# Performance work log

Measured on AMD Instinct MI355X. Metric: run time of the kernel, lower is better.

## Reference

```python
import jax, jax.numpy as jnp
import numpy as np

DIM = 128
POS_HID = 64
ATTN_HID = DIM * 4
K_NEIGH = 16


def _mlp2(x, w1, b1, w2, b2):
    # Linear -> ReLU -> Linear (weights stored as (in, out))
    return jax.nn.relu(x @ w1 + b1) @ w2 + b2


def setup_inputs() -> dict:
    key = jax.random.key(0)
    ks = jax.random.split(key, 12)
    B, N = 2, 512
    s = 0.05
    return {
        "x": jax.random.normal(ks[0], (B, DIM, N), jnp.float32),
        "pos": jax.random.normal(ks[1], (B, N, 3), jnp.float32),
        "w_qkv": jax.random.normal(ks[2], (DIM, 3 * DIM), jnp.float32) * s,
        "pos_w1": jax.random.normal(ks[3], (3, POS_HID), jnp.float32) * s,
        "pos_b1": jnp.zeros((POS_HID,), jnp.float32),
        "pos_w2": jax.random.normal(ks[4], (POS_HID, DIM), jnp.float32) * s,
        "pos_b2": jnp.zeros((DIM,), jnp.float32),
        "attn_w1": jax.random.normal(ks[5], (DIM, ATTN_HID), jnp.float32) * s,
        "attn_b1": jnp.zeros((ATTN_HID,), jnp.float32),
        "attn_w2": jax.random.normal(ks[6], (ATTN_HID, DIM), jnp.float32) * s,
        "attn_b2": jnp.zeros((DIM,), jnp.float32),
    }


def reference(x, pos, w_qkv, pos_w1, pos_b1, pos_w2, pos_b2,
              attn_w1, attn_b1, attn_w2, attn_b2):
    # x: (B, dim, N) -> (B, N, dim)
    xt = jnp.swapaxes(x, 1, 2)
    B, N, d = xt.shape

    qkv = xt @ w_qkv                           # (B, N, 3d), no bias
    q, k, v = jnp.split(qkv, 3, axis=-1)

    rel_pos = pos[:, :, None, :] - pos[:, None, :, :]          # (B, N, N, 3)
    rel_pos_emb = _mlp2(rel_pos, pos_w1, pos_b1, pos_w2, pos_b2)  # (B, N, N, d)
    qk_rel = q[:, :, None, :] - k[:, None, :, :]               # (B, N, N, d)

    # KNN: smallest euclidean rel distances per query point
    rel_dist = jnp.sqrt(jnp.sum(rel_pos * rel_pos, axis=-1))   # (B, N, N)
    _, idx = jax.lax.top_k(-rel_dist, K_NEIGH)                 # (B, N, K)

    idxe = idx[..., None]                                      # (B, N, K, 1)
    v_g = v[jnp.arange(B)[:, None, None], idx]                 # (B, N, K, d)
    qk_g = jnp.take_along_axis(qk_rel, idxe, axis=2)           # (B, N, K, d)
    pe_g = jnp.take_along_axis(rel_pos_emb, idxe, axis=2)      # (B, N, K, d)

    v_g = v_g + pe_g
    sim = _mlp2(qk_g + pe_g, attn_w1, attn_b1, attn_w2, attn_b2)  # (B, N, K, d)
    attn = jax.nn.softmax(sim, axis=-2)                        # softmax over neighbors
    agg = jnp.einsum('bikd,bikd->bid', attn, v_g)              # (B, N, d)
    return jnp.swapaxes(agg, 1, 2)                             # (B, d, N)
```

## Files before the change

kernel.cpp:

```cpp
#include <hip/hip_runtime.h>
#include <math.h>

#define DIM 128
#define N_PTS 512
#define K_NEIGH 16
#define POS_HID 64
#define ATTN_HID 512

typedef __attribute__((ext_vector_type(8))) short short8;
typedef __attribute__((ext_vector_type(4))) float f32x4;
typedef unsigned short us;
typedef unsigned long long ull;

__device__ __forceinline__ us f2b(float f) {
    unsigned int u = __builtin_bit_cast(unsigned int, f);
    u += 0x7fffu + ((u >> 16) & 1u);
    return (us)(u >> 16);
}

__device__ __forceinline__ ull shflx64(ull v, int m) {
    int lo = __shfl_xor((int)(unsigned int)v, m);
    int hi = __shfl_xor((int)(unsigned int)(v >> 32), m);
    return ((ull)(unsigned int)hi << 32) | (unsigned int)lo;
}

__global__ void pack_kernel(const float* __restrict__ wqkv,
                            const float* __restrict__ aw1,
                            const float* __restrict__ aw2,
                            const float* __restrict__ pw2,
                            us* __restrict__ p0, us* __restrict__ p1,
                            us* __restrict__ p2, us* __restrict__ p3) {
    int t = blockIdx.x * 256 + threadIdx.x;
    if (t < 49152) {
        int j = t & 7, l = (t >> 3) & 63, rem = t >> 9;
        int nt = rem % 24, ks = rem / 24;
        int k = ks * 32 + (l >> 4) * 8 + j, n = nt * 16 + (l & 15);
        p0[t] = f2b(wqkv[k * 384 + n]);
    } else if (t < 114688) {
        int u = t - 49152;
        int j = u & 7, l = (u >> 3) & 63, nt = (u >> 9) & 31, ks = u >> 14;
        int k = ks * 32 + (l >> 4) * 8 + j, n = nt * 16 + (l & 15);
        p1[u] = f2b(aw1[k * ATTN_HID + n]);
    } else if (t < 180224) {
        int u = t - 114688;
        int j = u & 7, l = (u >> 3) & 63, nt = (u >> 9) & 7, ch = u >> 12;
        int k = ch * 32 + (l >> 4) * 8 + j, n = nt * 16 + (l & 15);
        p2[u] = f2b(aw2[k * DIM + n]);
    } else if (t < 188416) {
        int u = t - 180224;
        int j = u & 7, l = (u >> 3) & 63, nt = (u >> 9) & 7, ks = u >> 12;
        int k = ks * 32 + (l >> 4) * 8 + j, n = nt * 16 + (l & 15);
        p3[u] = f2b(pw2[k * DIM + n]);
    }
}

__global__ __launch_bounds__(512)
void qkv_mfma_kernel(const float* __restrict__ x,
                     const us* __restrict__ p0,
                     float* __restrict__ qkv) {
    __shared__ __align__(16) us xA[16][136];
    const int tid = threadIdx.x;
    const int w = tid >> 6, lane = tid & 63, quad = lane >> 4, lq = lane & 15;
    const int n0 = blockIdx.x * 16;
    const int b = n0 >> 9, nn = n0 & (N_PTS - 1);
#pragma unroll
    for (int rr = 0; rr < 4; ++rr) {
        int id = rr * 512 + tid;
        int d = id >> 4, i = id & 15;
        xA[i][d] = f2b(x[(size_t)(b * DIM + d) * N_PTS + nn + i]);
    }
    __syncthreads();
    short8 a[4];
#pragma unroll
    for (int ks = 0; ks < 4; ++ks)
        a[ks] = *(const short8*)&xA[lq][ks * 32 + quad * 8];
#pragma unroll
    for (int i = 0; i < 3; ++i) {
        int nt = w * 3 + i;
        f32x4 acc = {0.f, 0.f, 0.f, 0.f};
#pragma unroll
        for (int ks = 0; ks < 4; ++ks) {
            const short8 bf = *(const short8*)(p0 + (size_t)((ks * 24 + nt) * 64 + lane) * 8);
            acc = __builtin_amdgcn_mfma_f32_16x16x32_bf16(a[ks], bf, acc, 0, 0, 0);
        }
#pragma unroll
        for (int r = 0; r < 4; ++r)
            qkv[(size_t)(n0 + quad * 4 + r) * 384 + nt * 16 + lq] = acc[r];
    }
}

__global__ __launch_bounds__(256, 1)
void attn_fused_kernel(const float* __restrict__ pos,
                       const float* __restrict__ qkv,
                       const float* __restrict__ pw1,
                       const float* __restrict__ pb1,
                       const float* __restrict__ pb2,
                       const us* __restrict__ p1,
                       const us* __restrict__ p2,
                       const us* __restrict__ p3,
                       const float* __restrict__ ab1,
                       float* __restrict__ out) {
    __shared__ __align__(16) us hinA[4][16][136];
    __shared__ __align__(16) us h1s[4][16][40];
    __shared__ int nbrs[4][16];

    const int tid = threadIdx.x;
    const int w = tid >> 6, lane = tid & 63, quad = lane >> 4, lq = lane & 15;
    const int g = blockIdx.x * 4 + w, b = g >> 9, n = g & (N_PTS - 1);

    short8 b3f[2][8];
#pragma unroll
    for (int ks = 0; ks < 2; ++ks)
#pragma unroll
        for (int nt = 0; nt < 8; ++nt)
            b3f[ks][nt] = *(const short8*)(p3 + (size_t)((ks * 8 + nt) * 64 + lane) * 8);

    float w1x[2][8], w1y[2][8], w1z[2][8], w1b[2][8];
#pragma unroll
    for (int ks = 0; ks < 2; ++ks)
#pragma unroll
        for (int jj = 0; jj < 8; ++jj) {
            int c = ks * 32 + quad * 8 + jj;
            w1x[ks][jj] = pw1[c];
            w1y[ks][jj] = pw1[64 + c];
            w1z[ks][jj] = pw1[128 + c];
            w1b[ks][jj] = pb1[c];
        }

    float qvr[8], pb2r[8], ab1r[32];
#pragma unroll
    for (int nt = 0; nt < 8; ++nt) {
        qvr[nt]  = qkv[(size_t)g * 384 + nt * 16 + lq];
        pb2r[nt] = pb2[nt * 16 + lq];
    }
#pragma unroll
    for (int nt = 0; nt < 32; ++nt) ab1r[nt] = ab1[nt * 16 + lq];

    {
        const float pix = pos[g * 3 + 0], piy = pos[g * 3 + 1], piz = pos[g * 3 + 2];
        float d2[8];
#pragma unroll
        for (int rr = 0; rr < 8; ++rr) {
            int j = rr * 64 + lane;
            float dx = pix - pos[(b * N_PTS + j) * 3 + 0];
            float dy = piy - pos[(b * N_PTS + j) * 3 + 1];
            float dz = piz - pos[(b * N_PTS + j) * 3 + 2];
            d2[rr] = dx * dx + dy * dy + dz * dz;
        }
        for (int r = 0; r < K_NEIGH; ++r) {
            ull key = ~0ULL;
#pragma unroll
            for (int rr = 0; rr < 8; ++rr) {
                unsigned int fb = __builtin_bit_cast(unsigned int, d2[rr]);
                ull k2 = ((ull)fb << 32) | (unsigned int)(rr * 64 + lane);
                key = k2 < key ? k2 : key;
            }
#pragma unroll
            for (int off = 32; off > 0; off >>= 1) {
                ull o = shflx64(key, off);
                key = o < key ? o : key;
            }
            unsigned int jw = (unsigned int)key;
            if (lane == 0) nbrs[w][r] = (int)jw;
            if (lane == (int)(jw & 63)) d2[jw >> 6] = __builtin_inff();
        }
    }

    short8 pha[2];
    {
        const int jn = nbrs[w][lq];
        float rx = pos[g * 3 + 0] - pos[(b * N_PTS + jn) * 3 + 0];
        float ry = pos[g * 3 + 1] - pos[(b * N_PTS + jn) * 3 + 1];
        float rz = pos[g * 3 + 2] - pos[(b * N_PTS + jn) * 3 + 2];
#pragma unroll
        for (int ks = 0; ks < 2; ++ks) {
            short8 f;
#pragma unroll
            for (int jj = 0; jj < 8; ++jj) {
                float h = rx * w1x[ks][jj] + ry * w1y[ks][jj] + rz * w1z[ks][jj] + w1b[ks][jj];
                f[jj] = (short)f2b(fmaxf(h, 0.f));
            }
            pha[ks] = f;
        }
    }

    f32x4 pe[8];
#pragma unroll
    for (int nt = 0; nt < 8; ++nt) {
        f32x4 acc = {0.f, 0.f, 0.f, 0.f};
        acc = __builtin_amdgcn_mfma_f32_16x16x32_bf16(pha[0], b3f[0][nt], acc, 0, 0, 0);
        acc = __builtin_amdgcn_mfma_f32_16x16x32_bf16(pha[1], b3f[1][nt], acc, 0, 0, 0);
#pragma unroll
        for (int r = 0; r < 4; ++r) pe[nt][r] = acc[r] + pb2r[nt];
    }

    f32x4 vg[8];
    {
        int jr[4];
#pragma unroll
        for (int r = 0; r < 4; ++r) jr[r] = nbrs[w][quad * 4 + r];
#pragma unroll
        for (int nt = 0; nt < 8; ++nt) {
            int d = nt * 16 + lq;
#pragma unroll
            for (int r = 0; r < 4; ++r) {
                const float* kv = qkv + (size_t)(b * N_PTS + jr[r]) * 384;
                float pp = pe[nt][r];
                hinA[w][quad * 4 + r][d] = f2b(qvr[nt] - kv[128 + d] + pp);
                vg[nt][r] = kv[256 + d] + pp;
            }
        }
    }

    short8 a1f[4];
#pragma unroll
    for (int ks = 0; ks < 4; ++ks)
        a1f[ks] = *(const short8*)&hinA[w][lq][ks * 32 + quad * 8];

    f32x4 c2[8];
#pragma unroll
    for (int nt = 0; nt < 8; ++nt) c2[nt] = (f32x4){0.f, 0.f, 0.f, 0.f};

    short8 p1f[2][2][4];
    short8 p2f[2][8];
#pragma unroll
    for (int t = 0; t < 2; ++t)
#pragma unroll
        for (int ks = 0; ks < 4; ++ks)
            p1f[0][t][ks] = *(const short8*)(p1 + (size_t)(((ks << 5) + t) * 64 + lane) * 8);
#pragma unroll
    for (int nt2 = 0; nt2 < 8; ++nt2)
        p2f[0][nt2] = *(const short8*)(p2 + (size_t)(nt2 * 64 + lane) * 8);

#pragma unroll
    for (int ch = 0; ch < 16; ++ch) {
        const int cur = ch & 1, nxt = cur ^ 1;
        if (ch < 15) {
#pragma unroll
            for (int t = 0; t < 2; ++t)
#pragma unroll
                for (int ks = 0; ks < 4; ++ks)
                    p1f[nxt][t][ks] = *(const short8*)(p1 + (size_t)(((ks << 5) + (ch + 1) * 2 + t) * 64 + lane) * 8);
        }
#pragma unroll
        for (int t = 0; t < 2; ++t) {
            int nt = ch * 2 + t;
            f32x4 acc = {0.f, 0.f, 0.f, 0.f};
#pragma unroll
            for (int ks = 0; ks < 4; ++ks)
                acc = __builtin_amdgcn_mfma_f32_16x16x32_bf16(a1f[ks], p1f[cur][t][ks], acc, 0, 0, 0);
            float bias = ab1r[nt];
#pragma unroll
            for (int r = 0; r < 4; ++r)
                h1s[w][quad * 4 + r][t * 16 + lq] = f2b(fmaxf(acc[r] + bias, 0.f));
        }
        if (ch < 15) {
#pragma unroll
            for (int nt2 = 0; nt2 < 8; ++nt2)
                p2f[nxt][nt2] = *(const short8*)(p2 + (size_t)((((ch + 1) << 3) + nt2) * 64 + lane) * 8);
        }
        const short8 a2 = *(const short8*)&h1s[w][lq][quad * 8];
#pragma unroll
        for (int nt2 = 0; nt2 < 8; ++nt2)
            c2[nt2] = __builtin_amdgcn_mfma_f32_16x16x32_bf16(a2, p2f[cur][nt2], c2[nt2], 0, 0, 0);
    }

#pragma unroll
    for (int nt2 = 0; nt2 < 8; ++nt2) {
        f32x4 s4 = c2[nt2];
        float m = fmaxf(fmaxf(s4[0], s4[1]), fmaxf(s4[2], s4[3]));
        m = fmaxf(m, __shfl_xor(m, 16));
        m = fmaxf(m, __shfl_xor(m, 32));
        float e0 = __expf(s4[0] - m), e1 = __expf(s4[1] - m);
        float e2 = __expf(s4[2] - m), e3 = __expf(s4[3] - m);
        float s = e0 + e1 + e2 + e3;
        f32x4 v4 = vg[nt2];
        float a = e0 * v4[0] + e1 * v4[1] + e2 * v4[2] + e3 * v4[3];
        s += __shfl_xor(s, 16); s += __shfl_xor(s, 32);
        a += __shfl_xor(a, 16); a += __shfl_xor(a, 32);
        if (quad == 0)
            out[(size_t)(b * DIM + nt2 * 16 + lq) * N_PTS + n] = a / s;
    }
}

extern "C" void kernel_launch(void* const* d_in, const int* in_sizes, int n_in,
                              void* d_out, int out_size, void* d_ws, size_t ws_size,
                              hipStream_t stream) {
    const float* x    = (const float*)d_in[0];
    const float* pos  = (const float*)d_in[1];
    const float* wqkv = (const float*)d_in[2];
    const float* pw1  = (const float*)d_in[3];
    const float* pb1  = (const float*)d_in[4];
    const float* pw2  = (const float*)d_in[5];
    const float* pb2  = (const float*)d_in[6];
    const float* aw1  = (const float*)d_in[7];
    const float* ab1  = (const float*)d_in[8];
    const float* aw2  = (const float*)d_in[9];
    float* out = (float*)d_out;

    int B = in_sizes[0] / (DIM * N_PTS);
    int npts = B * N_PTS;

    char* ws = (char*)d_ws;
    float* qkv = (float*)ws;
    us* p0 = (us*)(ws + (size_t)npts * 384 * 4);
    us* p1 = p0 + 49152;
    us* p2 = p1 + 65536;
    us* p3 = p2 + 65536;

    pack_kernel<<<736, 256, 0, stream>>>(wqkv, aw1, aw2, pw2, p0, p1, p2, p3);
    qkv_mfma_kernel<<<npts / 16, 512, 0, stream>>>(x, p0, qkv);
    attn_fused_kernel<<<npts / 4, 256, 0, stream>>>(pos, qkv,
                                                    pw1, pb1, pb2,
                                                    p1, p2, p3, ab1, out);
}
```

Measured before the change: 100.1 us.

## Split attention MLP hidden dimension across wave pairs with LDS reduction

Each point is now handled by two waves instead of one. Each wave computes half of the 512-wide hidden layer of the attention MLP, and the partial second-layer accumulators are exchanged through shared memory after a block barrier. Each wave then does the softmax and aggregation for half of the output channels. The grid doubles and launch bounds allow two blocks per CU, which aims to shorten the serial MFMA chain per wave and raise occupancy. The cost is that KNN selection and positional-embedding work are repeated in both waves, the register double-buffered weight prefetch is removed, and a __syncthreads plus LDS traffic is added.

```diff
diff --git a/kernel.cpp b/kernel.cpp
--- a/kernel.cpp
+++ b/kernel.cpp
@@ -89,7 +89,7 @@
     }
 }
 
-__global__ __launch_bounds__(256, 1)
+__global__ __launch_bounds__(256, 2)
 void attn_fused_kernel(const float* __restrict__ pos,
                        const float* __restrict__ qkv,
                        const float* __restrict__ pw1,
@@ -103,10 +103,13 @@
     __shared__ __align__(16) us hinA[4][16][136];
     __shared__ __align__(16) us h1s[4][16][40];
     __shared__ int nbrs[4][16];
+    __shared__ __align__(16) f32x4 cxch[4][4][64];
 
     const int tid = threadIdx.x;
     const int w = tid >> 6, lane = tid & 63, quad = lane >> 4, lq = lane & 15;
-    const int g = blockIdx.x * 4 + w, b = g >> 9, n = g & (N_PTS - 1);
+    const int pt = w >> 1, sub = w & 1;
+    const int g = blockIdx.x * 2 + pt, b = g >> 9, n = g & (N_PTS - 1);
+    const int ch0 = sub << 3;
 
     short8 b3f[2][8];
 #pragma unroll
@@ -127,14 +130,14 @@
             w1b[ks][jj] = pb1[c];
         }
 
-    float qvr[8], pb2r[8], ab1r[32];
+    float qvr[8], pb2r[8], ab1r[16];
 #pragma unroll
     for (int nt = 0; nt < 8; ++nt) {
         qvr[nt]  = qkv[(size_t)g * 384 + nt * 16 + lq];
         pb2r[nt] = pb2[nt * 16 + lq];
     }
 #pragma unroll
-    for (int nt = 0; nt < 32; ++nt) ab1r[nt] = ab1[nt * 16 + lq];
+    for (int i = 0; i < 16; ++i) ab1r[i] = ab1[(sub * 16 + i) * 16 + lq];
 
     {
         const float pix = pos[g * 3 + 0], piy = pos[g * 3 + 1], piz = pos[g * 3 + 2];
@@ -221,53 +224,48 @@
 #pragma unroll
     for (int nt = 0; nt < 8; ++nt) c2[nt] = (f32x4){0.f, 0.f, 0.f, 0.f};
 
-    short8 p1f[2][2][4];
-    short8 p2f[2][8];
-#pragma unroll
-    for (int t = 0; t < 2; ++t)
-#pragma unroll
-        for (int ks = 0; ks < 4; ++ks)
-            p1f[0][t][ks] = *(const short8*)(p1 + (size_t)(((ks << 5) + t) * 64 + lane) * 8);
-#pragma unroll
-    for (int nt2 = 0; nt2 < 8; ++nt2)
-        p2f[0][nt2] = *(const short8*)(p2 + (size_t)(nt2 * 64 + lane) * 8);
-
-#pragma unroll
-    for (int ch = 0; ch < 16; ++ch) {
-        const int cur = ch & 1, nxt = cur ^ 1;
-        if (ch < 15) {
-#pragma unroll
-            for (int t = 0; t < 2; ++t)
-#pragma unroll
-                for (int ks = 0; ks < 4; ++ks)
-                    p1f[nxt][t][ks] = *(const short8*)(p1 + (size_t)(((ks << 5) + (ch + 1) * 2 + t) * 64 + lane) * 8);
-        }
+#pragma unroll
+    for (int c = 0; c < 8; ++c) {
+        const int ch = ch0 + c;
+        short8 p1f[2][4];
+#pragma unroll
+        for (int t = 0; t < 2; ++t)
+#pragma unroll
+            for (int ks = 0; ks < 4; ++ks)
+                p1f[t][ks] = *(const short8*)(p1 + (size_t)(((ks << 5) + ch * 2 + t) * 64 + lane) * 8);
 #pragma unroll
         for (int t = 0; t < 2; ++t) {
-            int nt = ch * 2 + t;
             f32x4 acc = {0.f, 0.f, 0.f, 0.f};
 #pragma unroll
             for (int ks = 0; ks < 4; ++ks)
-                acc = __builtin_amdgcn_mfma_f32_16x16x32_bf16(a1f[ks], p1f[cur][t][ks], acc, 0, 0, 0);
-            float bias = ab1r[nt];
+                acc = __builtin_amdgcn_mfma_f32_16x16x32_bf16(a1f[ks], p1f[t][ks], acc, 0, 0, 0);
+            float bias = ab1r[c * 2 + t];
 #pragma unroll
             for (int r = 0; r < 4; ++r)
                 h1s[w][quad * 4 + r][t * 16 + lq] = f2b(fmaxf(acc[r] + bias, 0.f));
         }
-        if (ch < 15) {
-#pragma unroll
-            for (int nt2 = 0; nt2 < 8; ++nt2)
-                p2f[nxt][nt2] = *(const short8*)(p2 + (size_t)((((ch + 1) << 3) + nt2) * 64 + lane) * 8);
-        }
+        short8 p2f[8];
+#pragma unroll
+        for (int nt2 = 0; nt2 < 8; ++nt2)
+            p2f[nt2] = *(const short8*)(p2 + (size_t)(((ch << 3) + nt2) * 64 + lane) * 8);
         const short8 a2 = *(const short8*)&h1s[w][lq][quad * 8];
 #pragma unroll
         for (int nt2 = 0; nt2 < 8; ++nt2)
-            c2[nt2] = __builtin_amdgcn_mfma_f32_16x16x32_bf16(a2, p2f[cur][nt2], c2[nt2], 0, 0, 0);
-    }
-
-#pragma unroll
-    for (int nt2 = 0; nt2 < 8; ++nt2) {
+            c2[nt2] = __builtin_amdgcn_mfma_f32_16x16x32_bf16(a2, p2f[nt2], c2[nt2], 0, 0, 0);
+    }
+
+#pragma unroll
+    for (int i = 0; i < 4; ++i)
+        cxch[w][i][lane] = c2[(sub ^ 1) * 4 + i];
+    __syncthreads();
+
+#pragma unroll
+    for (int i = 0; i < 4; ++i) {
+        const int nt2 = sub * 4 + i;
+        f32x4 o = cxch[w ^ 1][i][lane];
         f32x4 s4 = c2[nt2];
+        s4[0] += o[0]; s4[1] += o[1]; s4[2] += o[2]; s4[3] += o[3];
+
         float m = fmaxf(fmaxf(s4[0], s4[1]), fmaxf(s4[2], s4[3]));
         m = fmaxf(m, __shfl_xor(m, 16));
         m = fmaxf(m, __shfl_xor(m, 32));
@@ -310,7 +308,7 @@
 
     pack_kernel<<<736, 256, 0, stream>>>(wqkv, aw1, aw2, pw2, p0, p1, p2, p3);
     qkv_mfma_kernel<<<npts / 16, 512, 0, stream>>>(x, p0, qkv);
-    attn_fused_kernel<<<npts / 4, 256, 0, stream>>>(pos, qkv,
+    attn_fused_kernel<<<npts / 2, 256, 0, stream>>>(pos, qkv,
                                                     pw1, pb1, pb2,
                                                     p1, p2, p3, ab1, out);
 }
```

New measurement: 111.4 us. 1.11x slower.

## Merge pack, QKV and attention kernels into one persistent kernel with grid barriers

Applied to the files above, without the earlier changes.

Replaces three separate launches (weight packing, QKV MFMA GEMM, fused attention) with a single kernel of npts/4 blocks that runs each phase in turn, separated by atomic-counter grid barriers. The aim is to remove launch gaps and inter-kernel drain between phases. The QKV work is redistributed so that four blocks share a 16-point tile, each computing six of the output column tiles. The grid barrier assumes all 256 blocks are co-resident, which holds on a 256-CU device with one block per CU but risks deadlock otherwise. It also adds a memset launch to reset the counters.

```diff
diff --git a/kernel.cpp b/kernel.cpp
--- a/kernel.cpp
+++ b/kernel.cpp
@@ -24,88 +24,103 @@
     return ((ull)(unsigned int)hi << 32) | (unsigned int)lo;
 }
 
-__global__ void pack_kernel(const float* __restrict__ wqkv,
-                            const float* __restrict__ aw1,
-                            const float* __restrict__ aw2,
-                            const float* __restrict__ pw2,
-                            us* __restrict__ p0, us* __restrict__ p1,
-                            us* __restrict__ p2, us* __restrict__ p3) {
-    int t = blockIdx.x * 256 + threadIdx.x;
-    if (t < 49152) {
-        int j = t & 7, l = (t >> 3) & 63, rem = t >> 9;
-        int nt = rem % 24, ks = rem / 24;
-        int k = ks * 32 + (l >> 4) * 8 + j, n = nt * 16 + (l & 15);
-        p0[t] = f2b(wqkv[k * 384 + n]);
-    } else if (t < 114688) {
-        int u = t - 49152;
-        int j = u & 7, l = (u >> 3) & 63, nt = (u >> 9) & 31, ks = u >> 14;
-        int k = ks * 32 + (l >> 4) * 8 + j, n = nt * 16 + (l & 15);
-        p1[u] = f2b(aw1[k * ATTN_HID + n]);
-    } else if (t < 180224) {
-        int u = t - 114688;
-        int j = u & 7, l = (u >> 3) & 63, nt = (u >> 9) & 7, ch = u >> 12;
-        int k = ch * 32 + (l >> 4) * 8 + j, n = nt * 16 + (l & 15);
-        p2[u] = f2b(aw2[k * DIM + n]);
-    } else if (t < 188416) {
-        int u = t - 180224;
-        int j = u & 7, l = (u >> 3) & 63, nt = (u >> 9) & 7, ks = u >> 12;
-        int k = ks * 32 + (l >> 4) * 8 + j, n = nt * 16 + (l & 15);
-        p3[u] = f2b(pw2[k * DIM + n]);
-    }
-}
-
-__global__ __launch_bounds__(512)
-void qkv_mfma_kernel(const float* __restrict__ x,
-                     const us* __restrict__ p0,
-                     float* __restrict__ qkv) {
+__device__ __forceinline__ void gbar(int* cnt, int target) {
+    __syncthreads();
+    if (threadIdx.x == 0) {
+        __hip_atomic_fetch_add(cnt, 1, __ATOMIC_RELEASE, __HIP_MEMORY_SCOPE_AGENT);
+        while (__hip_atomic_load(cnt, __ATOMIC_ACQUIRE, __HIP_MEMORY_SCOPE_AGENT) < target)
+            __builtin_amdgcn_s_sleep(2);
+    }
+    __syncthreads();
+}
+
+__global__ __launch_bounds__(256, 1)
+void fused_kernel(const float* __restrict__ x,
+                  const float* __restrict__ pos,
+                  const float* __restrict__ wqkv,
+                  const float* __restrict__ pw1,
+                  const float* __restrict__ pb1,
+                  const float* __restrict__ pw2,
+                  const float* __restrict__ pb2,
+                  const float* __restrict__ aw1,
+                  const float* __restrict__ ab1,
+                  const float* __restrict__ aw2,
+                  float* __restrict__ qkv,
+                  us* __restrict__ p0, us* __restrict__ p1,
+                  us* __restrict__ p2, us* __restrict__ p3,
+                  int* __restrict__ bar,
+                  float* __restrict__ out, int npts) {
     __shared__ __align__(16) us xA[16][136];
-    const int tid = threadIdx.x;
-    const int w = tid >> 6, lane = tid & 63, quad = lane >> 4, lq = lane & 15;
-    const int n0 = blockIdx.x * 16;
-    const int b = n0 >> 9, nn = n0 & (N_PTS - 1);
-#pragma unroll
-    for (int rr = 0; rr < 4; ++rr) {
-        int id = rr * 512 + tid;
-        int d = id >> 4, i = id & 15;
-        xA[i][d] = f2b(x[(size_t)(b * DIM + d) * N_PTS + nn + i]);
-    }
-    __syncthreads();
-    short8 a[4];
-#pragma unroll
-    for (int ks = 0; ks < 4; ++ks)
-        a[ks] = *(const short8*)&xA[lq][ks * 32 + quad * 8];
-#pragma unroll
-    for (int i = 0; i < 3; ++i) {
-        int nt = w * 3 + i;
-        f32x4 acc = {0.f, 0.f, 0.f, 0.f};
-#pragma unroll
-        for (int ks = 0; ks < 4; ++ks) {
-            const short8 bf = *(const short8*)(p0 + (size_t)((ks * 24 + nt) * 64 + lane) * 8);
-            acc = __builtin_amdgcn_mfma_f32_16x16x32_bf16(a[ks], bf, acc, 0, 0, 0);
-        }
-#pragma unroll
-        for (int r = 0; r < 4; ++r)
-            qkv[(size_t)(n0 + quad * 4 + r) * 384 + nt * 16 + lq] = acc[r];
-    }
-}
-
-__global__ __launch_bounds__(256, 1)
-void attn_fused_kernel(const float* __restrict__ pos,
-                       const float* __restrict__ qkv,
-                       const float* __restrict__ pw1,
-                       const float* __restrict__ pb1,
-                       const float* __restrict__ pb2,
-                       const us* __restrict__ p1,
-                       const us* __restrict__ p2,
-                       const us* __restrict__ p3,
-                       const float* __restrict__ ab1,
-                       float* __restrict__ out) {
     __shared__ __align__(16) us hinA[4][16][136];
     __shared__ __align__(16) us h1s[4][16][40];
     __shared__ int nbrs[4][16];
 
     const int tid = threadIdx.x;
     const int w = tid >> 6, lane = tid & 63, quad = lane >> 4, lq = lane & 15;
+    const int nblk = npts >> 2;
+
+    {
+        const int gsz = nblk * 256;
+        for (int t = blockIdx.x * 256 + tid; t < 188416; t += gsz) {
+            if (t < 49152) {
+                int j = t & 7, l = (t >> 3) & 63, rem = t >> 9;
+                int nt = rem % 24, ks = rem / 24;
+                int k = ks * 32 + (l >> 4) * 8 + j, n = nt * 16 + (l & 15);
+                p0[t] = f2b(wqkv[k * 384 + n]);
+            } else if (t < 114688) {
+                int u = t - 49152;
+                int j = u & 7, l = (u >> 3) & 63, nt = (u >> 9) & 31, ks = u >> 14;
+                int k = ks * 32 + (l >> 4) * 8 + j, n = nt * 16 + (l & 15);
+                p1[u] = f2b(aw1[k * ATTN_HID + n]);
+            } else if (t < 180224) {
+                int u = t - 114688;
+                int j = u & 7, l = (u >> 3) & 63, nt = (u >> 9) & 7, ch = u >> 12;
+                int k = ch * 32 + (l >> 4) * 8 + j, n = nt * 16 + (l & 15);
+                p2[u] = f2b(aw2[k * DIM + n]);
+            } else {
+                int u = t - 180224;
+                int j = u & 7, l = (u >> 3) & 63, nt = (u >> 9) & 7, ks = u >> 12;
+                int k = ks * 32 + (l >> 4) * 8 + j, n = nt * 16 + (l & 15);
+                p3[u] = f2b(pw2[k * DIM + n]);
+            }
+        }
+    }
+    gbar(&bar[0], nblk);
+
+    {
+        const int n0 = (blockIdx.x >> 2) * 16;
+        const int ntb = (blockIdx.x & 3) * 6;
+        const int b = n0 >> 9, nn = n0 & (N_PTS - 1);
+#pragma unroll
+        for (int rr = 0; rr < 8; ++rr) {
+            int id = rr * 256 + tid;
+            int d = id >> 4, i = id & 15;
+            xA[i][d] = f2b(x[(size_t)(b * DIM + d) * N_PTS + nn + i]);
+        }
+        __syncthreads();
+        short8 a[4];
+#pragma unroll
+        for (int ks = 0; ks < 4; ++ks)
+            a[ks] = *(const short8*)&xA[lq][ks * 32 + quad * 8];
+#pragma unroll
+        for (int i = 0; i < 2; ++i) {
+            int nl = w + i * 4;
+            if (nl < 6) {
+                int nt = ntb + nl;
+                f32x4 acc = {0.f, 0.f, 0.f, 0.f};
+#pragma unroll
+                for (int ks = 0; ks < 4; ++ks) {
+                    const short8 bf = *(const short8*)(p0 + (size_t)((ks * 24 + nt) * 64 + lane) * 8);
+                    acc = __builtin_amdgcn_mfma_f32_16x16x32_bf16(a[ks], bf, acc, 0, 0, 0);
+                }
+#pragma unroll
+                for (int r = 0; r < 4; ++r)
+                    qkv[(size_t)(n0 + quad * 4 + r) * 384 + nt * 16 + lq] = acc[r];
+            }
+        }
+    }
+    gbar(&bar[1], nblk);
+
     const int g = blockIdx.x * 4 + w, b = g >> 9, n = g & (N_PTS - 1);
 
     short8 b3f[2][8];
@@ -307,10 +322,10 @@
     us* p1 = p0 + 49152;
     us* p2 = p1 + 65536;
     us* p3 = p2 + 65536;
-
-    pack_kernel<<<736, 256, 0, stream>>>(wqkv, aw1, aw2, pw2, p0, p1, p2, p3);
-    qkv_mfma_kernel<<<npts / 16, 512, 0, stream>>>(x, p0, qkv);
-    attn_fused_kernel<<<npts / 4, 256, 0, stream>>>(pos, qkv,
-                                                    pw1, pb1, pb2,
-                                                    p1, p2, p3, ab1, out);
-}
+    int* bar = (int*)(ws + (size_t)4 * 1024 * 1024);
+
+    hipMemsetAsync(bar, 0, 2 * sizeof(int), stream);
+    fused_kernel<<<npts / 4, 256, 0, stream>>>(x, pos, wqkv, pw1, pb1, pw2,
+                                               pb2, aw1, ab1, aw2, qkv,
+                                               p0, p1, p2, p3, bar, out, npts);
+}
```

Result: slower. 121.9 us (+21.8%).

## Split attention kernel into KNN/pos-embedding and MLP kernels; widen QKV grid

Applied to the files above, without the earlier changes.

The fused attention kernel is split in two. The first kernel does the KNN selection and the positional-embedding MLP, writing neighbor indices and embeddings (npts*16*128 floats) to workspace. The second kernel reads them back and runs the attention MLP and aggregation, with fewer registers live per kernel. The QKV projection now launches 4x more blocks of 256 threads, each handling 6 output tiles, to raise occupancy. The cost is an extra launch and a global-memory round trip for the embeddings.

```diff
diff --git a/kernel.cpp b/kernel.cpp
--- a/kernel.cpp
+++ b/kernel.cpp
@@ -54,18 +54,19 @@
     }
 }
 
-__global__ __launch_bounds__(512)
+__global__ __launch_bounds__(256)
 void qkv_mfma_kernel(const float* __restrict__ x,
                      const us* __restrict__ p0,
                      float* __restrict__ qkv) {
     __shared__ __align__(16) us xA[16][136];
     const int tid = threadIdx.x;
     const int w = tid >> 6, lane = tid & 63, quad = lane >> 4, lq = lane & 15;
-    const int n0 = blockIdx.x * 16;
+    const int n0 = (blockIdx.x >> 2) * 16;
+    const int ntb = (blockIdx.x & 3) * 6;
     const int b = n0 >> 9, nn = n0 & (N_PTS - 1);
 #pragma unroll
-    for (int rr = 0; rr < 4; ++rr) {
-        int id = rr * 512 + tid;
+    for (int rr = 0; rr < 8; ++rr) {
+        int id = rr * 256 + tid;
         int d = id >> 4, i = id & 15;
         xA[i][d] = f2b(x[(size_t)(b * DIM + d) * N_PTS + nn + i]);
     }
@@ -75,38 +76,34 @@
     for (int ks = 0; ks < 4; ++ks)
         a[ks] = *(const short8*)&xA[lq][ks * 32 + quad * 8];
 #pragma unroll
-    for (int i = 0; i < 3; ++i) {
-        int nt = w * 3 + i;
-        f32x4 acc = {0.f, 0.f, 0.f, 0.f};
-#pragma unroll
-        for (int ks = 0; ks < 4; ++ks) {
-            const short8 bf = *(const short8*)(p0 + (size_t)((ks * 24 + nt) * 64 + lane) * 8);
-            acc = __builtin_amdgcn_mfma_f32_16x16x32_bf16(a[ks], bf, acc, 0, 0, 0);
-        }
-#pragma unroll
-        for (int r = 0; r < 4; ++r)
-            qkv[(size_t)(n0 + quad * 4 + r) * 384 + nt * 16 + lq] = acc[r];
+    for (int i = 0; i < 2; ++i) {
+        int nl = w + i * 4;
+        if (nl < 6) {
+            int nt = ntb + nl;
+            f32x4 acc = {0.f, 0.f, 0.f, 0.f};
+#pragma unroll
+            for (int ks = 0; ks < 4; ++ks) {
+                const short8 bf = *(const short8*)(p0 + (size_t)((ks * 24 + nt) * 64 + lane) * 8);
+                acc = __builtin_amdgcn_mfma_f32_16x16x32_bf16(a[ks], bf, acc, 0, 0, 0);
+            }
+#pragma unroll
+            for (int r = 0; r < 4; ++r)
+                qkv[(size_t)(n0 + quad * 4 + r) * 384 + nt * 16 + lq] = acc[r];
+        }
     }
 }
 
 __global__ __launch_bounds__(256, 1)
-void attn_fused_kernel(const float* __restrict__ pos,
-                       const float* __restrict__ qkv,
-                       const float* __restrict__ pw1,
-                       const float* __restrict__ pb1,
-                       const float* __restrict__ pb2,
-                       const us* __restrict__ p1,
-                       const us* __restrict__ p2,
-                       const us* __restrict__ p3,
-                       const float* __restrict__ ab1,
-                       float* __restrict__ out) {
-    __shared__ __align__(16) us hinA[4][16][136];
-    __shared__ __align__(16) us h1s[4][16][40];
-    __shared__ int nbrs[4][16];
-
+void attn_pre_kernel(const float* __restrict__ pos,
+                     const float* __restrict__ pw1,
+                     const float* __restrict__ pb1,
+                     const float* __restrict__ pb2,
+                     const us* __restrict__ p3,
+                     int* __restrict__ nbr_ws,
+                     float* __restrict__ pe_ws) {
     const int tid = threadIdx.x;
     const int w = tid >> 6, lane = tid & 63, quad = lane >> 4, lq = lane & 15;
-    const int g = blockIdx.x * 4 + w, b = g >> 9, n = g & (N_PTS - 1);
+    const int g = blockIdx.x * 4 + w, b = g >> 9;
 
     short8 b3f[2][8];
 #pragma unroll
@@ -126,16 +123,11 @@
             w1z[ks][jj] = pw1[128 + c];
             w1b[ks][jj] = pb1[c];
         }
-
-    float qvr[8], pb2r[8], ab1r[32];
-#pragma unroll
-    for (int nt = 0; nt < 8; ++nt) {
-        qvr[nt]  = qkv[(size_t)g * 384 + nt * 16 + lq];
-        pb2r[nt] = pb2[nt * 16 + lq];
-    }
-#pragma unroll
-    for (int nt = 0; nt < 32; ++nt) ab1r[nt] = ab1[nt * 16 + lq];
-
+    float pb2r[8];
+#pragma unroll
+    for (int nt = 0; nt < 8; ++nt) pb2r[nt] = pb2[nt * 16 + lq];
+
+    int jn = 0;
     {
         const float pix = pos[g * 3 + 0], piy = pos[g * 3 + 1], piz = pos[g * 3 + 2];
         float d2[8];
@@ -161,14 +153,14 @@
                 key = o < key ? o : key;
             }
             unsigned int jw = (unsigned int)key;
-            if (lane == 0) nbrs[w][r] = (int)jw;
+            if (r == lq) jn = (int)jw;
             if (lane == (int)(jw & 63)) d2[jw >> 6] = __builtin_inff();
         }
     }
+    if (lane < 16) nbr_ws[g * 16 + lane] = jn;
 
     short8 pha[2];
     {
-        const int jn = nbrs[w][lq];
         float rx = pos[g * 3 + 0] - pos[(b * N_PTS + jn) * 3 + 0];
         float ry = pos[g * 3 + 1] - pos[(b * N_PTS + jn) * 3 + 1];
         float rz = pos[g * 3 + 2] - pos[(b * N_PTS + jn) * 3 + 2];
@@ -184,31 +176,52 @@
         }
     }
 
-    f32x4 pe[8];
 #pragma unroll
     for (int nt = 0; nt < 8; ++nt) {
         f32x4 acc = {0.f, 0.f, 0.f, 0.f};
         acc = __builtin_amdgcn_mfma_f32_16x16x32_bf16(pha[0], b3f[0][nt], acc, 0, 0, 0);
         acc = __builtin_amdgcn_mfma_f32_16x16x32_bf16(pha[1], b3f[1][nt], acc, 0, 0, 0);
 #pragma unroll
-        for (int r = 0; r < 4; ++r) pe[nt][r] = acc[r] + pb2r[nt];
-    }
+        for (int r = 0; r < 4; ++r)
+            pe_ws[((size_t)g * 16 + quad * 4 + r) * 128 + nt * 16 + lq] = acc[r] + pb2r[nt];
+    }
+}
+
+__global__ __launch_bounds__(256, 1)
+void attn_mlp_kernel(const float* __restrict__ qkv,
+                     const us* __restrict__ p1,
+                     const us* __restrict__ p2,
+                     const float* __restrict__ ab1,
+                     const int* __restrict__ nbr_ws,
+                     const float* __restrict__ pe_ws,
+                     float* __restrict__ out) {
+    __shared__ __align__(16) us hinA[4][16][136];
+    __shared__ __align__(16) us h1s[4][16][40];
+
+    const int tid = threadIdx.x;
+    const int w = tid >> 6, lane = tid & 63, quad = lane >> 4, lq = lane & 15;
+    const int g = blockIdx.x * 4 + w, b = g >> 9, n = g & (N_PTS - 1);
+
+    float qvr[8], ab1r[32];
+#pragma unroll
+    for (int nt = 0; nt < 8; ++nt) qvr[nt] = qkv[(size_t)g * 384 + nt * 16 + lq];
+#pragma unroll
+    for (int nt = 0; nt < 32; ++nt) ab1r[nt] = ab1[nt * 16 + lq];
+
+    int jr[4];
+#pragma unroll
+    for (int r = 0; r < 4; ++r) jr[r] = nbr_ws[g * 16 + quad * 4 + r];
 
     f32x4 vg[8];
-    {
-        int jr[4];
-#pragma unroll
-        for (int r = 0; r < 4; ++r) jr[r] = nbrs[w][quad * 4 + r];
-#pragma unroll
-        for (int nt = 0; nt < 8; ++nt) {
-            int d = nt * 16 + lq;
-#pragma unroll
-            for (int r = 0; r < 4; ++r) {
-                const float* kv = qkv + (size_t)(b * N_PTS + jr[r]) * 384;
-                float pp = pe[nt][r];
-                hinA[w][quad * 4 + r][d] = f2b(qvr[nt] - kv[128 + d] + pp);
-                vg[nt][r] = kv[256 + d] + pp;
-            }
+#pragma unroll
+    for (int nt = 0; nt < 8; ++nt) {
+        int d = nt * 16 + lq;
+#pragma unroll
+        for (int r = 0; r < 4; ++r) {
+            const float* kv = qkv + (size_t)(b * N_PTS + jr[r]) * 384;
+            float pp = pe_ws[((size_t)g * 16 + quad * 4 + r) * 128 + d];
+            hinA[w][quad * 4 + r][d] = f2b(qvr[nt] - kv[128 + d] + pp);
+            vg[nt][r] = kv[256 + d] + pp;
         }
     }
 
@@ -307,10 +320,13 @@
     us* p1 = p0 + 49152;
     us* p2 = p1 + 65536;
     us* p3 = p2 + 65536;
+    int*   nbr_ws = (int*)  (ws + (size_t)2 * 1024 * 1024);
+    float* pe_ws  = (float*)(ws + (size_t)4 * 1024 * 1024);
 
     pack_kernel<<<736, 256, 0, stream>>>(wqkv, aw1, aw2, pw2, p0, p1, p2, p3);
-    qkv_mfma_kernel<<<npts / 16, 512, 0, stream>>>(x, p0, qkv);
-    attn_fused_kernel<<<npts / 4, 256, 0, stream>>>(pos, qkv,
-                                                    pw1, pb1, pb2,
-                                                    p1, p2, p3, ab1, out);
-}
+    qkv_mfma_kernel<<<npts / 4, 256, 0, stream>>>(x, p0, qkv);
+    attn_pre_kernel<<<npts / 4, 256, 0, stream>>>(pos, pw1, pb1, pb2, p3,
+                                                  nbr_ws, pe_ws);
+    attn_mlp_kernel<<<npts / 4, 256, 0, stream>>>(qkv, p1, p2, ab1,
+                                                  nbr_ws, pe_ws, out);
+}
```

After: 124.1 us. +24.0%, slower.
